# Kernel optimization log

Measured on AMD Instinct MI355X. Metric: run time of the kernel, lower is better.

Reference implementation:

```python
import jax, jax.numpy as jnp
import numpy as np

B, S, DIN, H, DOUT, E, SEL = 8, 2048, 512, 512, 512, 262144, 512
N = B * S


def setup_inputs() -> dict:
    key = jax.random.key(0)
    ks = jax.random.split(key, 20)
    inp = {
        "x": jax.random.normal(ks[0], (B, S, DIN), dtype=jnp.float32),
        "edge_index": jax.random.randint(ks[1], (2, E), 0, N, dtype=jnp.int64),
        "selected_idx": jax.random.randint(ks[2], (B, SEL), 0, S, dtype=jnp.int64),
        "edge_label": jax.random.randint(ks[3], (E,), 0, 8, dtype=jnp.int64),
    }
    k = 4
    for l, fin in enumerate([DIN, H, H]):
        inp[f"conv{l}_w1"] = jax.random.normal(ks[k], (2 * fin, H), dtype=jnp.float32) * 0.02; k += 1
        inp[f"conv{l}_b1"] = jnp.full((H,), 0.01, dtype=jnp.float32)
        inp[f"conv{l}_w2"] = jax.random.normal(ks[k], (H, H), dtype=jnp.float32) * 0.02; k += 1
        inp[f"conv{l}_b2"] = jnp.full((H,), 0.01, dtype=jnp.float32)
    inp["ffn_w1"] = jax.random.normal(ks[k], (H, H), dtype=jnp.float32) * 0.02; k += 1
    inp["ffn_b1"] = jnp.full((H,), 0.01, dtype=jnp.float32)
    inp["ffn_w2"] = jax.random.normal(ks[k], (H, DOUT), dtype=jnp.float32) * 0.02; k += 1
    inp["ffn_b2"] = jnp.full((DOUT,), 0.01, dtype=jnp.float32)
    return inp


def _ffw(x, w1, b1, w2, b2):
    # FeedForward: fc2(act_dropout(relu(fc1(x)))), dropout=0 in eval
    return jax.nn.relu(x @ w1 + b1) @ w2 + b2


def reference(x, edge_index, selected_idx, edge_label,
              conv0_w1, conv0_b1, conv0_w2, conv0_b2,
              conv1_w1, conv1_b1, conv1_w2, conv1_b2,
              conv2_w1, conv2_b1, conv2_w2, conv2_b2,
              ffn_w1, ffn_b1, ffn_w2, ffn_b2):
    b, s, d = x.shape
    n = b * s
    h = x.reshape(n, d)
    src, dst = edge_index[0], edge_index[1]  # PyG: x_j = source, x_i = target
    convs = [(conv0_w1, conv0_b1, conv0_w2, conv0_b2),
             (conv1_w1, conv1_b1, conv1_w2, conv1_b2),
             (conv2_w1, conv2_b1, conv2_w2, conv2_b2)]
    for w1, b1, w2, b2 in convs:
        xi = h[dst]                                   # [E, F]
        xj = h[src]
        ef = jnp.concatenate([xi, xj - xi], axis=1)   # [E, 2F]
        m = _ffw(ef, w1, b1, w2, b2)                  # per-edge MLP [E, H]
        agg = jax.ops.segment_max(m, dst, num_segments=n)
        agg = jnp.where(jnp.isneginf(agg), 0.0, agg)  # empty segments -> 0 (PyG fill)
        h = jax.nn.relu(agg)                          # dropout p acts as identity in eval
    h = _ffw(h, ffn_w1, ffn_b1, ffn_w2, ffn_b2)
    out = h.reshape(b, s, -1)                         # [B, S, DOUT]
    idx = jnp.broadcast_to(selected_idx[:, :, None], (b, selected_idx.shape[1], out.shape[-1]))
    return jnp.take_along_axis(out, idx, axis=1)      # [B, SEL, DOUT]
```

## Files before the change

kernel.cpp:

```cpp
#include <hip/hip_runtime.h>
#include <hip/hip_bf16.h>


#define N_NODES 16384
#define EDGES   262144
#define HDIM    512
#define SEQ     2048

typedef __attribute__((ext_vector_type(8))) short short8;
typedef __attribute__((ext_vector_type(8))) _Float16 half8;
typedef __attribute__((ext_vector_type(2))) _Float16 half2v;
typedef __attribute__((ext_vector_type(4))) float f32x4;

__device__ __forceinline__ void gld16(const void* g, void* l) {
    __builtin_amdgcn_global_load_lds(
        (const __attribute__((address_space(1))) void*)g,
        (__attribute__((address_space(3))) void*)l, 16, 0, 0);
}
__device__ __forceinline__ unsigned short f2b(float f) {
    unsigned int x = __float_as_uint(f);
    return (unsigned short)((x + 0x7fffu + ((x >> 16) & 1u)) >> 16);
}
__device__ __forceinline__ unsigned short f2h(float f) {
    _Float16 h = (_Float16)f;
    return __builtin_bit_cast(unsigned short, h);
}
__device__ __forceinline__ unsigned int zpack_h(unsigned int u, unsigned int v) {
    half2v a = __builtin_bit_cast(half2v, u);
    half2v b = __builtin_bit_cast(half2v, v);
    half2v s = a + b;
    half2v z = {(_Float16)0.f, (_Float16)0.f};
    half2v r = __builtin_elementwise_max(s, z);
    return __builtin_bit_cast(unsigned int, r);
}
__device__ __forceinline__ short8 frag_ld(const short* S, int row, int q) {
    int p = q ^ ((row >> 1) & 3);
    return *(const short8*)(S + row * 32 + p * 8);
}
__device__ __forceinline__ void stage_tile(const short* G, int kc, short* S, int t) {
#pragma unroll
    for (int it = 0; it < 2; ++it) {
        int lin = it * 256 + t;
        int row = lin >> 2, p = lin & 3;
        int q = p ^ ((row >> 1) & 3);
        gld16(G + (size_t)row * HDIM + kc + q * 8, S + lin * 8);
    }
}
__device__ __forceinline__ void mfma_tile_bf16(const short* As, const short* Bs,
                                               int wm, int wn, int l, f32x4 acc[4][4]) {
    short8 a[4], b[4];
#pragma unroll
    for (int mt = 0; mt < 4; ++mt) a[mt] = frag_ld(As, wm + mt * 16 + (l & 15), l >> 4);
#pragma unroll
    for (int nt = 0; nt < 4; ++nt) b[nt] = frag_ld(Bs, wn + nt * 16 + (l & 15), l >> 4);
#pragma unroll
    for (int mt = 0; mt < 4; ++mt)
#pragma unroll
        for (int nt = 0; nt < 4; ++nt)
            acc[mt][nt] = __builtin_amdgcn_mfma_f32_16x16x32_bf16(a[mt], b[nt], acc[mt][nt], 0, 0, 0);
}
__device__ __forceinline__ half8 frag64(const short* S, int row, int q) {
    int p = q ^ ((row >> 1) & 7) ^ (row & 1);
    return *(const half8*)(S + row * 64 + p * 8);
}
__device__ __forceinline__ void stageB32w(const short* __restrict__ Wt, int col0,
                                          short* buf, int t) {
#pragma unroll
    for (int it = 0; it < 4; ++it) {
        int lin = it * 512 + t;
        int row = lin >> 2, s = lin & 3;
        int q = s ^ ((row >> 1) & 3);
        gld16(Wt + (size_t)row * HDIM + col0 + q * 8, buf + lin * 8);
    }
}

__global__ __launch_bounds__(256) void hist_kernel(
    const int* __restrict__ dst, int* __restrict__ hist) {
    int idx = blockIdx.x * 256 + threadIdx.x;
    atomicAdd(&hist[dst[idx]], 1);
}
__global__ __launch_bounds__(256) void scan_kernel(
    const int* __restrict__ hist, int* __restrict__ cursor) {
    __shared__ int part[256];
    const int t = threadIdx.x, base = t * 64;
    int sum = 0;
    for (int i = 0; i < 64; ++i) sum += hist[base + i];
    part[t] = sum;
    __syncthreads();
    int run = 0;
    for (int i = 0; i < t; ++i) run += part[i];
    for (int i = 0; i < 64; ++i) {
        int h = hist[base + i];
        cursor[base + i] = run;
        run += h;
    }
}
__global__ __launch_bounds__(256) void scatter_kernel(
    const int* __restrict__ dst, const int* __restrict__ src,
    int* __restrict__ cursor, int* __restrict__ dstS, int* __restrict__ srcS) {
    int idx = blockIdx.x * 256 + threadIdx.x;
    int d = dst[idx];
    int p = atomicAdd(&cursor[d], 1);
    dstS[p] = d;
    srcS[p] = src[idx];
}

__global__ __launch_bounds__(256) void prep_weights_kernel(
    const float* __restrict__ w1, const float* __restrict__ w2,
    short* __restrict__ WdT, short* __restrict__ w1bT, short* __restrict__ W2T) {
    __shared__ float tile[32][33];
    const int which = blockIdx.z;
    const int k0 = blockIdx.x * 32, n0 = blockIdx.y * 32;
    const int tx = threadIdx.x, ty = threadIdx.y;
#pragma unroll
    for (int i = 0; i < 4; ++i) {
        int k = k0 + ty + i * 8, n = n0 + tx;
        float v;
        if (which == 0)      v = w1[k * 512 + n] - w1[(k + 512) * 512 + n];
        else if (which == 1) v = w1[(k + 512) * 512 + n];
        else                 v = w2[k * 512 + n];
        tile[ty + i * 8][tx] = v;
    }
    __syncthreads();
    short* out = which == 0 ? WdT : (which == 1 ? w1bT : W2T);
#pragma unroll
    for (int i = 0; i < 4; ++i) {
        int n = n0 + ty + i * 8, k = k0 + tx;
        float v = tile[tx][ty + i * 8];
        out[(size_t)n * 512 + k] = (short)(which == 2 ? f2h(v) : f2b(v));
    }
}
__global__ __launch_bounds__(256) void tr_kernel(
    const float* __restrict__ W1, const float* __restrict__ W2,
    short* __restrict__ T1, short* __restrict__ T2) {
    __shared__ float tile[32][33];
    const float* W = blockIdx.z ? W2 : W1;
    short* T = blockIdx.z ? T2 : T1;
    const int k0 = blockIdx.x * 32, n0 = blockIdx.y * 32;
    const int tx = threadIdx.x, ty = threadIdx.y;
#pragma unroll
    for (int i = 0; i < 4; ++i)
        tile[ty + i * 8][tx] = W[(k0 + ty + i * 8) * 512 + n0 + tx];
    __syncthreads();
#pragma unroll
    for (int i = 0; i < 4; ++i)
        T[(size_t)(n0 + ty + i * 8) * 512 + k0 + tx] = (short)f2b(tile[tx][ty + i * 8]);
}
__global__ __launch_bounds__(256) void cvt_bf16_kernel(
    const float* __restrict__ x, short* __restrict__ xb) {
    int idx = blockIdx.x * 256 + threadIdx.x;
    float4 v = ((const float4*)x)[idx];
    uint2 o;
    o.x = (unsigned int)f2b(v.x) | ((unsigned int)f2b(v.y) << 16);
    o.y = (unsigned int)f2b(v.z) | ((unsigned int)f2b(v.w) << 16);
    ((uint2*)xb)[idx] = o;
}

__global__ __launch_bounds__(256) void node_gemm_uv_kernel(
    const short* __restrict__ A, const short* __restrict__ WdT,
    const short* __restrict__ w1bT, const float* __restrict__ b1,
    short* __restrict__ U, short* __restrict__ V) {
    __shared__ short As[128 * 32];
    __shared__ short Bs[128 * 32];
    const int t = threadIdx.x;
    const int by = blockIdx.y;
    const short* Wt = (by < 4) ? WdT : w1bT;
    short* C = (by < 4) ? U : V;
    const float* bias = (by < 4) ? b1 : nullptr;
    const int m0 = blockIdx.x * 128, n0 = (by & 3) * 128;
    const int w = t >> 6, l = t & 63;
    const int wm = (w & 1) * 64, wn = (w >> 1) * 64;
    f32x4 acc[4][4] = {};
    for (int kc = 0; kc < HDIM; kc += 32) {
        stage_tile(A + (size_t)m0 * HDIM, kc, As, t);
        stage_tile(Wt + (size_t)n0 * HDIM, kc, Bs, t);
        __syncthreads();
        mfma_tile_bf16(As, Bs, wm, wn, l, acc);
        __syncthreads();
    }
#pragma unroll
    for (int mt = 0; mt < 4; ++mt) {
        int m = m0 + wm + mt * 16 + (l >> 4) * 4;
#pragma unroll
        for (int nt = 0; nt < 4; ++nt) {
            int n = n0 + wn + nt * 16 + (l & 15);
            float bv = bias ? bias[n] : 0.f;
#pragma unroll
            for (int r = 0; r < 4; ++r)
                C[(size_t)(m + r) * HDIM + n] = (short)f2h(acc[mt][nt][r] + bv);
        }
    }
}

__device__ __forceinline__ unsigned int fkey(float m) {
    unsigned int b = __float_as_uint(m);
    return ((int)b < 0) ? ~b : (b | 0x80000000u);
}
__device__ __forceinline__ void kflush(unsigned int* K, int d, int col, float m) {
    atomicMax(K + (((size_t)d) << 9) + col, fkey(m));
}
__global__ __launch_bounds__(512, 4) void edge_mfma_kernel(
    const short* __restrict__ U, const short* __restrict__ V,
    const short* __restrict__ Wt, const int* __restrict__ srcS,
    const int* __restrict__ dstS, unsigned int* __restrict__ K) {
    __shared__ short As[64 * 64];
    __shared__ short Bs[2][512 * 32];
    const int t = threadIdx.x;
    const int L  = blockIdx.x;
    const int g  = (L & 7) * 512 + (L >> 3);
    const int e0 = g * 64;
    const int w = t >> 6, l = t & 63;
    const int wnb = w * 64;
    const int lm = l & 15;
    const int arow = t >> 3, s0 = t & 7;
    const int perm = ((arow >> 1) & 7) ^ (arow & 1);
    const int p0 = s0 ^ perm;
    const int drow = dstS[e0 + arow];
    const int srow = srcS[e0 + arow];
    const short* up = U + (((size_t)drow) << 9) + s0 * 8;
    const short* vp = V + (((size_t)srow) << 9) + s0 * 8;
    unsigned int* As_u = (unsigned int*)As;
    f32x4 acc[4][4] = {};
    uint4 pu0, pv0;
    stageB32w(Wt, 0, Bs[0], t);
    pu0 = *(const uint4*)(up);
    pv0 = *(const uint4*)(vp);
#pragma unroll
    for (int hh = 0; hh < 16; ++hh) {
        const int kc = (hh >> 1) * 64;
        if (hh < 15) {
            const int c1 = ((hh + 1) >> 1) * 64 + ((hh + 1) & 1) * 32;
            stageB32w(Wt, c1, Bs[(hh + 1) & 1], t);
        }
        if ((hh & 1) == 0) {
            uint4 z0;
            z0.x = zpack_h(pu0.x, pv0.x); z0.y = zpack_h(pu0.y, pv0.y);
            z0.z = zpack_h(pu0.z, pv0.z); z0.w = zpack_h(pu0.w, pv0.w);
            *(uint4*)(As_u + arow * 32 + p0 * 4) = z0;
            if (hh < 14) {
                pu0 = *(const uint4*)(up + kc + 64);
                pv0 = *(const uint4*)(vp + kc + 64);
            }
        }
        if (hh < 14)       asm volatile("s_waitcnt vmcnt(6) lgkmcnt(0)" ::: "memory");
        else if (hh == 14) asm volatile("s_waitcnt vmcnt(4) lgkmcnt(0)" ::: "memory");
        else               asm volatile("s_waitcnt vmcnt(0) lgkmcnt(0)" ::: "memory");
        __builtin_amdgcn_s_barrier();
        asm volatile("" ::: "memory");
        const short* Bb = Bs[hh & 1];
        const int hq = (hh & 1) * 4 + (l >> 4);
        __builtin_amdgcn_s_setprio(1);
        half8 b[4];
#pragma unroll
        for (int nt = 0; nt < 4; ++nt) {
            int row = wnb + nt * 16 + lm;
            int p = (l >> 4) ^ ((row >> 1) & 3);
            b[nt] = *(const half8*)(Bb + row * 32 + p * 8);
        }
#pragma unroll
        for (int mt = 0; mt < 4; ++mt) {
            half8 a = frag64(As, mt * 16 + lm, hq);
#pragma unroll
            for (int nt = 0; nt < 4; ++nt)
                acc[mt][nt] = __builtin_amdgcn_mfma_f32_16x16x32_f16(a, b[nt], acc[mt][nt], 0, 0, 0);
        }
        __builtin_amdgcn_s_setprio(0);
        asm volatile("" ::: "memory");
        __builtin_amdgcn_s_barrier();
    }
    const int dbase = dstS[e0];
    const int drange = dstS[e0 + 63] - dbase + 1;
    unsigned int* tile = (unsigned int*)Bs[0];
    if (drange <= 16) {
        uint4 zz = {0u, 0u, 0u, 0u};
#pragma unroll
        for (int i = 0; i < 4; ++i) ((uint4*)tile)[i * 512 + t] = zz;
        __syncthreads();
#pragma unroll
        for (int mt = 0; mt < 4; ++mt) {
            int base = mt * 16 + (l >> 4) * 4;
            const int4 dd = *(const int4*)(dstS + e0 + base);
            int r0 = dd.x - dbase, r1 = dd.y - dbase, r2 = dd.z - dbase, r3 = dd.w - dbase;
#pragma unroll
            for (int nt = 0; nt < 4; ++nt) {
                int colb = wnb + nt * 16 + lm;
                f32x4 a = acc[mt][nt];
                float m = a[0];
                if (r1 == r0) m = fmaxf(m, a[1]);
                else { atomicMax(tile + r0 * 512 + colb, fkey(m)); m = a[1]; }
                if (r2 == r1) m = fmaxf(m, a[2]);
                else { atomicMax(tile + r1 * 512 + colb, fkey(m)); m = a[2]; }
                if (r3 == r2) m = fmaxf(m, a[3]);
                else { atomicMax(tile + r2 * 512 + colb, fkey(m)); m = a[3]; }
                atomicMax(tile + r3 * 512 + colb, fkey(m));
            }
        }
        __syncthreads();
#pragma unroll 4
        for (int r = 0; r < 16; ++r) {
            if (r < drange) {
                unsigned int kv = tile[r * 512 + t];
                if (kv) {
                    unsigned int* addr = K + (((size_t)(dbase + r)) << 9) + t;
                    if (r > 0 && r < drange - 1) *addr = kv;
                    else atomicMax(addr, kv);
                }
            }
        }
    } else {
#pragma unroll
        for (int mt = 0; mt < 4; ++mt) {
            int base = mt * 16 + (l >> 4) * 4;
            const int4 dd = *(const int4*)(dstS + e0 + base);
            int d0 = dd.x, d1 = dd.y, d2 = dd.z, d3 = dd.w;
#pragma unroll
            for (int nt = 0; nt < 4; ++nt) {
                int col = wnb + nt * 16 + lm;
                f32x4 a = acc[mt][nt];
                float m = a[0];
                if (d1 == d0) m = fmaxf(m, a[1]); else { kflush(K, d0, col, m); m = a[1]; }
                if (d2 == d1) m = fmaxf(m, a[2]); else { kflush(K, d1, col, m); m = a[2]; }
                if (d3 == d2) m = fmaxf(m, a[3]); else { kflush(K, d2, col, m); m = a[3]; }
                kflush(K, d3, col, m);
            }
        }
    }
}

__global__ __launch_bounds__(256) void decode_kernel(
    unsigned int* __restrict__ K, const float* __restrict__ b2,
    short* __restrict__ hb) {
    int idx = blockIdx.x * 256 + threadIdx.x;
    unsigned int k = K[idx];
    K[idx] = 0u;
    int c = idx & (HDIM - 1);
    float v = 0.f;
    if (k != 0u) {
        unsigned int b = (k & 0x80000000u) ? (k ^ 0x80000000u) : ~k;
        v = __uint_as_float(b) + b2[c];
    }
    hb[idx] = (short)f2b(fmaxf(v, 0.f));
}

__global__ __launch_bounds__(256) void gather_bf16_kernel(
    const short* __restrict__ hb, const int* __restrict__ sel,
    short* __restrict__ hgb) {
    int idx = blockIdx.x * 256 + threadIdx.x;
    int row = idx >> 6, c = idx & 63;
    int b = row >> 9;
    int s = sel[row];
    ((uint4*)hgb)[idx] = ((const uint4*)(hb + (((size_t)(b * SEQ + s)) << 9)))[c];
}

__global__ __launch_bounds__(256) void ffn_gemm_kernel(
    const short* __restrict__ A, const short* __restrict__ Wt,
    const float* __restrict__ bias, short* __restrict__ Cb,
    float* __restrict__ Cf, int relu) {
    __shared__ short As[128 * 32];
    __shared__ short Bs[128 * 32];
    const int t = threadIdx.x;
    const int m0 = blockIdx.x * 128, n0 = blockIdx.y * 128;
    const int w = t >> 6, l = t & 63;
    const int wm = (w & 1) * 64, wn = (w >> 1) * 64;
    f32x4 acc[4][4] = {};
    for (int kc = 0; kc < HDIM; kc += 32) {
        stage_tile(A + (size_t)m0 * HDIM, kc, As, t);
        stage_tile(Wt + (size_t)n0 * HDIM, kc, Bs, t);
        __syncthreads();
        mfma_tile_bf16(As, Bs, wm, wn, l, acc);
        __syncthreads();
    }
#pragma unroll
    for (int mt = 0; mt < 4; ++mt) {
        int m = m0 + wm + mt * 16 + (l >> 4) * 4;
#pragma unroll
        for (int nt = 0; nt < 4; ++nt) {
            int n = n0 + wn + nt * 16 + (l & 15);
            float bv = bias[n];
#pragma unroll
            for (int r = 0; r < 4; ++r) {
                float v = acc[mt][nt][r] + bv;
                if (relu) v = fmaxf(v, 0.f);
                if (Cf) Cf[(size_t)(m + r) * HDIM + n] = v;
                else    Cb[(size_t)(m + r) * HDIM + n] = (short)f2b(v);
            }
        }
    }
}

extern "C" void kernel_launch(void* const* d_in, const int* in_sizes, int n_in,
                              void* d_out, int out_size, void* d_ws, size_t ws_size,
                              hipStream_t stream) {
    const float* x   = (const float*)d_in[0];
    const int*   ei  = (const int*)d_in[1];
    const int*   sel = (const int*)d_in[2];
    const int*   src = ei;
    const int*   dst = ei + EDGES;
    const float* cw1[3] = {(const float*)d_in[4],  (const float*)d_in[8],  (const float*)d_in[12]};
    const float* cb1[3] = {(const float*)d_in[5],  (const float*)d_in[9],  (const float*)d_in[13]};
    const float* cw2[3] = {(const float*)d_in[6],  (const float*)d_in[10], (const float*)d_in[14]};
    const float* cb2[3] = {(const float*)d_in[7],  (const float*)d_in[11], (const float*)d_in[15]};
    const float* fw1 = (const float*)d_in[16];
    const float* fb1 = (const float*)d_in[17];
    const float* fw2 = (const float*)d_in[18];
    const float* fb2 = (const float*)d_in[19];
    float* out = (float*)d_out;

    const size_t MB = 1024 * 1024;
    char* p = (char*)d_ws;
    unsigned int* keys = (unsigned int*)p;
    short* U    = (short*)(p + 32 * MB);
    short* V    = (short*)(p + 48 * MB);
    short* hb   = (short*)(p + 64 * MB);
    short* WdT  = (short*)(p + 80 * MB);
    short* w1bT = WdT + 512 * 512;
    short* W2T  = w1bT + 512 * 512;
    short* fw1T = W2T + 512 * 512;
    short* fw2T = fw1T + 512 * 512;
    int*   dstS = (int*)(p + 83 * MB);
    int*   srcS = (int*)(p + 84 * MB);
    int*   hist = (int*)(p + 85 * MB);
    int*   curs = hist + N_NODES;
    short* hgb  = (short*)(p + 86 * MB);
    short* t1b  = (short*)(p + 90 * MB);

    (void)hipMemsetAsync(hist, 0, N_NODES * sizeof(int), stream);
    hist_kernel<<<EDGES / 256, 256, 0, stream>>>(dst, hist);
    scan_kernel<<<1, 256, 0, stream>>>(hist, curs);
    scatter_kernel<<<EDGES / 256, 256, 0, stream>>>(dst, src, curs, dstS, srcS);

    cvt_bf16_kernel<<<8192, 256, 0, stream>>>(x, hb);
    tr_kernel<<<dim3(16, 16, 2), dim3(32, 8), 0, stream>>>(fw1, fw2, fw1T, fw2T);
    (void)hipMemsetAsync(keys, 0, 32 * MB, stream);

    for (int l = 0; l < 3; ++l) {
        prep_weights_kernel<<<dim3(16, 16, 3), dim3(32, 8), 0, stream>>>(
            cw1[l], cw2[l], WdT, w1bT, W2T);
        node_gemm_uv_kernel<<<dim3(128, 8), 256, 0, stream>>>(hb, WdT, w1bT, cb1[l], U, V);
        edge_mfma_kernel<<<4096, 512, 0, stream>>>(U, V, W2T, srcS, dstS, keys);
        decode_kernel<<<(N_NODES * HDIM) / 256, 256, 0, stream>>>(keys, cb2[l], hb);
    }

    gather_bf16_kernel<<<(4096 * 64) / 256, 256, 0, stream>>>(hb, sel, hgb);
    ffn_gemm_kernel<<<dim3(32, 4), 256, 0, stream>>>(hgb, fw1T, fb1, t1b, nullptr, 1);
    ffn_gemm_kernel<<<dim3(32, 4), 256, 0, stream>>>(t1b, fw2T, fb2, nullptr, out, 0);
}
```

Measured before the change: 870.3 us.

## Halve edge MLP kernel threads, doubling per-wave N tile to 128 columns

The edge MFMA kernel now runs with 256 threads (4 waves) per block instead of 512 (8 waves). Each wave covers 128 output columns with an accumulator of 4x8 f32x4. Each thread does twice as many staging loads and A-tile writes, and the s_waitcnt counts are adjusted to match. The goal is to raise A-fragment reuse per wave and cut barrier and sync overhead. The cost is much higher register pressure, fewer waves per CU, and less latency hiding.

```diff
diff --git a/kernel.cpp b/kernel.cpp
--- a/kernel.cpp
+++ b/kernel.cpp
@@ -63,11 +63,11 @@
     int p = q ^ ((row >> 1) & 7) ^ (row & 1);
     return *(const half8*)(S + row * 64 + p * 8);
 }
-__device__ __forceinline__ void stageB32w(const short* __restrict__ Wt, int col0,
+__device__ __forceinline__ void stageB32n(const short* __restrict__ Wt, int col0,
                                           short* buf, int t) {
 #pragma unroll
-    for (int it = 0; it < 4; ++it) {
-        int lin = it * 512 + t;
+    for (int it = 0; it < 8; ++it) {
+        int lin = it * 256 + t;
         int row = lin >> 2, s = lin & 3;
         int q = s ^ ((row >> 1) & 3);
         gld16(Wt + (size_t)row * HDIM + col0 + q * 8, buf + lin * 8);
@@ -199,7 +199,7 @@
 __device__ __forceinline__ void kflush(unsigned int* K, int d, int col, float m) {
     atomicMax(K + (((size_t)d) << 9) + col, fkey(m));
 }
-__global__ __launch_bounds__(512, 4) void edge_mfma_kernel(
+__global__ __launch_bounds__(256, 2) void edge_mfma_kernel(
     const short* __restrict__ U, const short* __restrict__ V,
     const short* __restrict__ Wt, const int* __restrict__ srcS,
     const int* __restrict__ dstS, unsigned int* __restrict__ K) {
@@ -210,49 +210,56 @@
     const int g  = (L & 7) * 512 + (L >> 3);
     const int e0 = g * 64;
     const int w = t >> 6, l = t & 63;
-    const int wnb = w * 64;
+    const int wnb = w * 128;
     const int lm = l & 15;
-    const int arow = t >> 3, s0 = t & 7;
+    const int arow = t >> 2, s0 = (t & 3) * 2;
     const int perm = ((arow >> 1) & 7) ^ (arow & 1);
-    const int p0 = s0 ^ perm;
+    const int p0 = s0 ^ perm, p1 = (s0 + 1) ^ perm;
     const int drow = dstS[e0 + arow];
     const int srow = srcS[e0 + arow];
     const short* up = U + (((size_t)drow) << 9) + s0 * 8;
     const short* vp = V + (((size_t)srow) << 9) + s0 * 8;
     unsigned int* As_u = (unsigned int*)As;
-    f32x4 acc[4][4] = {};
-    uint4 pu0, pv0;
-    stageB32w(Wt, 0, Bs[0], t);
+    f32x4 acc[4][8] = {};
+    uint4 pu0, pu1, pv0, pv1;
+    stageB32n(Wt, 0, Bs[0], t);
     pu0 = *(const uint4*)(up);
+    pu1 = *(const uint4*)(up + 8);
     pv0 = *(const uint4*)(vp);
+    pv1 = *(const uint4*)(vp + 8);
 #pragma unroll
     for (int hh = 0; hh < 16; ++hh) {
         const int kc = (hh >> 1) * 64;
         if (hh < 15) {
             const int c1 = ((hh + 1) >> 1) * 64 + ((hh + 1) & 1) * 32;
-            stageB32w(Wt, c1, Bs[(hh + 1) & 1], t);
+            stageB32n(Wt, c1, Bs[(hh + 1) & 1], t);
         }
         if ((hh & 1) == 0) {
-            uint4 z0;
+            uint4 z0, z1;
             z0.x = zpack_h(pu0.x, pv0.x); z0.y = zpack_h(pu0.y, pv0.y);
             z0.z = zpack_h(pu0.z, pv0.z); z0.w = zpack_h(pu0.w, pv0.w);
+            z1.x = zpack_h(pu1.x, pv1.x); z1.y = zpack_h(pu1.y, pv1.y);
+            z1.z = zpack_h(pu1.z, pv1.z); z1.w = zpack_h(pu1.w, pv1.w);
             *(uint4*)(As_u + arow * 32 + p0 * 4) = z0;
+            *(uint4*)(As_u + arow * 32 + p1 * 4) = z1;
             if (hh < 14) {
                 pu0 = *(const uint4*)(up + kc + 64);
+                pu1 = *(const uint4*)(up + kc + 64 + 8);
                 pv0 = *(const uint4*)(vp + kc + 64);
+                pv1 = *(const uint4*)(vp + kc + 64 + 8);
             }
         }
-        if (hh < 14)       asm volatile("s_waitcnt vmcnt(6) lgkmcnt(0)" ::: "memory");
-        else if (hh == 14) asm volatile("s_waitcnt vmcnt(4) lgkmcnt(0)" ::: "memory");
+        if (hh <= 13)      asm volatile("s_waitcnt vmcnt(12) lgkmcnt(0)" ::: "memory");
+        else if (hh == 14) asm volatile("s_waitcnt vmcnt(8) lgkmcnt(0)" ::: "memory");
         else               asm volatile("s_waitcnt vmcnt(0) lgkmcnt(0)" ::: "memory");
         __builtin_amdgcn_s_barrier();
         asm volatile("" ::: "memory");
         const short* Bb = Bs[hh & 1];
         const int hq = (hh & 1) * 4 + (l >> 4);
         __builtin_amdgcn_s_setprio(1);
-        half8 b[4];
-#pragma unroll
-        for (int nt = 0; nt < 4; ++nt) {
+        half8 b[8];
+#pragma unroll
+        for (int nt = 0; nt < 8; ++nt) {
             int row = wnb + nt * 16 + lm;
             int p = (l >> 4) ^ ((row >> 1) & 3);
             b[nt] = *(const half8*)(Bb + row * 32 + p * 8);
@@ -261,7 +268,7 @@
         for (int mt = 0; mt < 4; ++mt) {
             half8 a = frag64(As, mt * 16 + lm, hq);
 #pragma unroll
-            for (int nt = 0; nt < 4; ++nt)
+            for (int nt = 0; nt < 8; ++nt)
                 acc[mt][nt] = __builtin_amdgcn_mfma_f32_16x16x32_f16(a, b[nt], acc[mt][nt], 0, 0, 0);
         }
         __builtin_amdgcn_s_setprio(0);
@@ -274,7 +281,7 @@
     if (drange <= 16) {
         uint4 zz = {0u, 0u, 0u, 0u};
 #pragma unroll
-        for (int i = 0; i < 4; ++i) ((uint4*)tile)[i * 512 + t] = zz;
+        for (int i = 0; i < 8; ++i) ((uint4*)tile)[i * 256 + t] = zz;
         __syncthreads();
 #pragma unroll
         for (int mt = 0; mt < 4; ++mt) {
@@ -282,7 +289,7 @@
             const int4 dd = *(const int4*)(dstS + e0 + base);
             int r0 = dd.x - dbase, r1 = dd.y - dbase, r2 = dd.z - dbase, r3 = dd.w - dbase;
 #pragma unroll
-            for (int nt = 0; nt < 4; ++nt) {
+            for (int nt = 0; nt < 8; ++nt) {
                 int colb = wnb + nt * 16 + lm;
                 f32x4 a = acc[mt][nt];
                 float m = a[0];
@@ -299,12 +306,12 @@
 #pragma unroll 4
         for (int r = 0; r < 16; ++r) {
             if (r < drange) {
-                unsigned int kv = tile[r * 512 + t];
-                if (kv) {
-                    unsigned int* addr = K + (((size_t)(dbase + r)) << 9) + t;
-                    if (r > 0 && r < drange - 1) *addr = kv;
-                    else atomicMax(addr, kv);
-                }
+                unsigned int kv0 = tile[r * 512 + t];
+                unsigned int kv1 = tile[r * 512 + 256 + t];
+                unsigned int* rowp = K + (((size_t)(dbase + r)) << 9);
+                bool interior = (r > 0 && r < drange - 1);
+                if (kv0) { if (interior) rowp[t] = kv0; else atomicMax(rowp + t, kv0); }
+                if (kv1) { if (interior) rowp[256 + t] = kv1; else atomicMax(rowp + 256 + t, kv1); }
             }
         }
     } else {
@@ -314,7 +321,7 @@
             const int4 dd = *(const int4*)(dstS + e0 + base);
             int d0 = dd.x, d1 = dd.y, d2 = dd.z, d3 = dd.w;
 #pragma unroll
-            for (int nt = 0; nt < 4; ++nt) {
+            for (int nt = 0; nt < 8; ++nt) {
                 int col = wnb + nt * 16 + lm;
                 f32x4 a = acc[mt][nt];
                 float m = a[0];
@@ -437,7 +444,7 @@
         prep_weights_kernel<<<dim3(16, 16, 3), dim3(32, 8), 0, stream>>>(
             cw1[l], cw2[l], WdT, w1bT, W2T);
         node_gemm_uv_kernel<<<dim3(128, 8), 256, 0, stream>>>(hb, WdT, w1bT, cb1[l], U, V);
-        edge_mfma_kernel<<<4096, 512, 0, stream>>>(U, V, W2T, srcS, dstS, keys);
+        edge_mfma_kernel<<<4096, 256, 0, stream>>>(U, V, W2T, srcS, dstS, keys);
         decode_kernel<<<(N_NODES * HDIM) / 256, 256, 0, stream>>>(keys, cb2[l], hb);
     }
 
```

After: 907.4 us. 4.3% more time.
